# Kernel tuning notes

Measured on AMD Instinct MI355X. Metric: run time of the kernel, lower is better.

## Reference

```python
import jax, jax.numpy as jnp
import numpy as np

B = 16        # batch
N = 1024      # satellite nodes
D = 256       # hidden size
H = 8         # attention heads
NUM_LAYERS = 3          # config.n_layer_aa
L = NUM_LAYERS + 1      # distinct GAT layers
EPS = 1e-5


def setup_inputs() -> dict:
    key = jax.random.key(0)
    ks = jax.random.split(key, 6)
    graph_vectors = jax.random.normal(ks[0], (B, N + 1, D), dtype=jnp.float32)
    graph = jax.random.uniform(ks[1], (B, N, N), dtype=jnp.float32)
    scale = 0.02
    Wq = jax.random.normal(ks[2], (L, D, D), dtype=jnp.float32) * scale
    Wk = jax.random.normal(ks[3], (L, D, D), dtype=jnp.float32) * scale
    Wv = jax.random.normal(ks[4], (L, D, D), dtype=jnp.float32) * scale
    Wo = jax.random.normal(ks[5], (L, D, D), dtype=jnp.float32) * scale
    ln_g = jnp.ones((L, D), dtype=jnp.float32)
    ln_b = jnp.zeros((L, D), dtype=jnp.float32)
    return {"graph_vectors": graph_vectors, "graph": graph,
            "Wq": Wq, "Wk": Wk, "Wv": Wv, "Wo": Wo,
            "ln_g": ln_g, "ln_b": ln_b}


def _layer_norm(x, g, b):
    mu = jnp.mean(x, axis=-1, keepdims=True)
    var = jnp.var(x, axis=-1, keepdims=True)
    return (x - mu) * jax.lax.rsqrt(var + EPS) * g + b


def _gat(x_q, x_kv, wq, wk, wv, wo, g, b):
    # multi-head attention: x_q [B,Lq,D] attends over x_kv [B,Lk,D]
    Bq, Lq, _ = x_q.shape
    Lk = x_kv.shape[1]
    dh = D // H
    q = (x_q @ wq).reshape(Bq, Lq, H, dh)
    k = (x_kv @ wk).reshape(Bq, Lk, H, dh)
    v = (x_kv @ wv).reshape(Bq, Lk, H, dh)
    scores = jnp.einsum('bqhd,bkhd->bhqk', q, k) / jnp.sqrt(jnp.float32(dh))
    attn = jax.nn.softmax(scores, axis=-1)
    o = jnp.einsum('bhqk,bkhd->bqhd', attn, v).reshape(Bq, Lq, D)
    out = o @ wo
    return _layer_norm(out + x_q, g, b)


def reference(graph_vectors, graph, Wq, Wk, Wv, Wo, ln_g, ln_b):
    relay = graph_vectors[:, :1, :]        # [B,1,D]
    sat = graph_vectors[:, 1:, :]          # [B,N,D]
    # layer 0: relay attends over satellites
    relay = _gat(relay, sat, Wq[0], Wk[0], Wv[0], Wo[0], ln_g[0], ln_b[0])
    # satellite = (satellite^T @ graph)^T -> [B,N,D]
    sat = jnp.einsum('bnd,bnm->bmd', sat, graph)
    gv = jnp.concatenate([relay, sat], axis=1)   # [B,N+1,D]
    # middle layers: full self-attention over all N+1 nodes
    for i in range(1, NUM_LAYERS):
        gv = _gat(gv, gv, Wq[i], Wk[i], Wv[i], Wo[i], ln_g[i], ln_b[i])
    relay_u = gv[:, :1, :]
    sat_u = gv[:, 1:, :]
    z = _gat(relay_u, sat_u, Wq[-1], Wk[-1], Wv[-1], Wo[-1], ln_g[-1], ln_b[-1])[:, 0, :]
    return z, sat_u
```

## Files before the change

### kernel.cpp

```cpp
#include <hip/hip_runtime.h>
#include <hip/hip_bf16.h>
#include <math.h>

#define BD   256
#define NH   8
#define DH   32
#define NB   16
#define NN   1024
#define LQ   1025
#define EPSV 1e-5f
#define KP   1088

typedef unsigned short ushort_t;
typedef __attribute__((ext_vector_type(8))) short short8;
typedef __attribute__((ext_vector_type(4))) float f32x4;

static __device__ __forceinline__ ushort_t f2b(float x) {
  union { __hip_bfloat16 h; ushort_t u; } cv;
  cv.h = __float2bfloat16(x);
  return cv.u;
}
static __device__ __forceinline__ float b2f(ushort_t u) {
  union { float f; unsigned v; } c; c.v = ((unsigned)u) << 16; return c.f;
}
static __device__ __forceinline__ float fexp2(float x) {
#if defined(__has_builtin)
#if __has_builtin(__builtin_amdgcn_exp2f)
  return __builtin_amdgcn_exp2f(x);
#else
  return exp2f(x);
#endif
#else
  return exp2f(x);
#endif
}

__global__ void k_copy_cast(const float* __restrict__ in, float* __restrict__ X,
                            ushort_t* __restrict__ Xh, long n) {
  long stride = (long)gridDim.x * 256;
  for (long i = (long)blockIdx.x * 256 + threadIdx.x; i < n; i += stride) {
    float v = in[i];
    X[i] = v;
    Xh[i] = f2b(v);
  }
}

__global__ void k_sat_out(const float* __restrict__ X, float* __restrict__ out) {
  long n = (long)NB * NN * BD;
  long stride = (long)gridDim.x * 256;
  for (long i = (long)blockIdx.x * 256 + threadIdx.x; i < n; i += stride) {
    long b = i / ((long)NN * BD);
    long r = i - b * ((long)NN * BD);
    out[i] = X[b * (long)LQ * BD + BD + r];
  }
}

__global__ __launch_bounds__(256) void k_wtrans(const float* __restrict__ Wq,
                                                const float* __restrict__ Wk,
                                                const float* __restrict__ Wv,
                                                const float* __restrict__ Wo,
                                                ushort_t* __restrict__ Wt) {
  const float C1 = 0.17677669529663687f * 1.4426950408889634f;
  int mat = blockIdx.y;
  int type = mat >> 2, layer = mat & 3;
  const float* src = (type == 0) ? Wq : (type == 1) ? Wk : (type == 2) ? Wv : Wo;
  src += (long)layer * BD * BD;
  float scv = (type == 0) ? C1 : 1.f;
  ushort_t* dst = Wt + (long)mat * BD * BD;
  __shared__ float t[32][33];
  int k0 = (blockIdx.x & 7) * 32, n0 = (blockIdx.x >> 3) * 32;
  int tid = threadIdx.x;
  for (int i = tid; i < 1024; i += 256) {
    int kk = i >> 5, nn = i & 31;
    t[kk][nn] = src[(long)(k0 + kk) * BD + n0 + nn];
  }
  __syncthreads();
  for (int i = tid; i < 1024; i += 256) {
    int nn = i >> 5, kk = i & 31;
    dst[(long)(n0 + nn) * BD + k0 + kk] = f2b(t[kk][nn] * scv);
  }
}

__global__ __launch_bounds__(256) void k_gtrans(const float* __restrict__ G,
                                                ushort_t* __restrict__ Ght) {
  __shared__ ushort_t t[64][65];
  int b = blockIdx.y;
  int m0 = (blockIdx.x & 15) * 64, n0 = (blockIdx.x >> 4) * 64;
  const float* Gb = G + (long)b * NN * NN;
  ushort_t* dst = Ght + (long)b * NN * NN;
  int tid = threadIdx.x;
  #pragma unroll
  for (int rr = 0; rr < 16; rr++) {
    int n = rr * 4 + (tid >> 6);
    int m = tid & 63;
    t[m][n] = f2b(Gb[(long)(n0 + n) * NN + m0 + m]);
  }
  __syncthreads();
  #pragma unroll
  for (int rr = 0; rr < 8; rr++) {
    int m = rr * 8 + (tid >> 5);
    int n2 = (tid & 31) * 2;
    unsigned w = (unsigned)t[m][n2] | ((unsigned)t[m][n2 + 1] << 16);
    *(unsigned*)&dst[(long)(m0 + m) * NN + n0 + n2] = w;
  }
}

__global__ __launch_bounds__(256) void k_satT(const ushort_t* __restrict__ Xh,
                                              ushort_t* __restrict__ satT) {
  __shared__ ushort_t t[64][65];
  int b = blockIdx.y;
  int n0 = (blockIdx.x & 15) * 64, d0 = (blockIdx.x >> 4) * 64;
  const ushort_t* src = Xh + ((long)b * LQ + 1) * BD;
  ushort_t* dst = satT + (long)b * BD * NN;
  int tid = threadIdx.x;
  #pragma unroll
  for (int rr = 0; rr < 16; rr++) {
    int n = rr * 4 + (tid >> 6);
    int d = tid & 63;
    t[n][d] = src[(long)(n0 + n) * BD + d0 + d];
  }
  __syncthreads();
  #pragma unroll
  for (int rr = 0; rr < 8; rr++) {
    int d = rr * 8 + (tid >> 5);
    int n2 = (tid & 31) * 2;
    unsigned w = (unsigned)t[n2][d] | ((unsigned)t[n2 + 1][d] << 16);
    *(unsigned*)&dst[(long)(d0 + d) * NN + n0 + n2] = w;
  }
}

__global__ __launch_bounds__(256) void k_vtrans(const ushort_t* __restrict__ Vh,
                                                ushort_t* __restrict__ VhT) {
  __shared__ ushort_t t[64][65];
  int b = blockIdx.z;
  int n0 = blockIdx.x * 64, d0 = blockIdx.y * 64;
  const ushort_t* src = Vh + (long)b * LQ * BD;
  ushort_t* dst = VhT + (long)b * BD * KP;
  int tid = threadIdx.x;
  #pragma unroll
  for (int rr = 0; rr < 16; rr++) {
    int n = rr * 4 + (tid >> 6);
    int d = tid & 63;
    int key = n0 + n;
    t[n][d] = (key < LQ) ? src[(long)key * BD + d0 + d] : (ushort_t)0;
  }
  __syncthreads();
  #pragma unroll
  for (int rr = 0; rr < 8; rr++) {
    int d = rr * 8 + (tid >> 5);
    int n2 = (tid & 31) * 2;
    unsigned w = (unsigned)t[n2][d] | ((unsigned)t[n2 + 1][d] << 16);
    *(unsigned*)&dst[(long)(d0 + d) * KP + n0 + n2] = w;
  }
}

static __device__ __forceinline__ void gemm_core(const ushort_t* __restrict__ A,
                                                 const ushort_t* __restrict__ W,
                                                 ushort_t* Ws,
                                                 float* __restrict__ Cf,
                                                 ushort_t* __restrict__ Ch,
                                                 int M, int m0, int n0) {
  int tid = threadIdx.x;
  int wave = tid >> 6, lane = tid & 63;
  int l15 = lane & 15, quad = lane >> 4;
  for (int i = tid; i < 64 * 32; i += 256) {
    int r = i >> 5, c8 = (i & 31) * 8;
    *(uint4*)&Ws[r * 264 + c8] = *(const uint4*)&W[(long)(n0 + r) * 256 + c8];
  }
  __syncthreads();
  int mrow = m0 + wave * 16 + l15;
  if (mrow > M - 1) mrow = M - 1;
  f32x4 acc[4];
  #pragma unroll
  for (int f = 0; f < 4; f++) { acc[f][0] = 0.f; acc[f][1] = 0.f; acc[f][2] = 0.f; acc[f][3] = 0.f; }
  #pragma unroll
  for (int k0 = 0; k0 < 256; k0 += 32) {
    short8 a = *(const short8*)&A[(long)mrow * 256 + k0 + quad * 8];
    #pragma unroll
    for (int f = 0; f < 4; f++) {
      short8 bb = *(const short8*)&Ws[(f * 16 + l15) * 264 + k0 + quad * 8];
      acc[f] = __builtin_amdgcn_mfma_f32_16x16x32_bf16(a, bb, acc[f], 0, 0, 0);
    }
  }
  #pragma unroll
  for (int f = 0; f < 4; f++)
    #pragma unroll
    for (int r = 0; r < 4; r++) {
      int m = m0 + wave * 16 + quad * 4 + r;
      if (m < M) {
        long idx = (long)m * 256 + n0 + f * 16 + l15;
        if (Cf) Cf[idx] = acc[f][r];
        else    Ch[idx] = f2b(acc[f][r]);
      }
    }
}

__global__ __launch_bounds__(256) void gemm_qkv(const ushort_t* __restrict__ Xh,
                                                const ushort_t* __restrict__ Wt, int layer,
                                                ushort_t* __restrict__ Qo,
                                                ushort_t* __restrict__ Ko,
                                                ushort_t* __restrict__ Vo, int M) {
  __shared__ __align__(16) ushort_t Ws[64 * 264];
  int which = blockIdx.y >> 2, n0 = (blockIdx.y & 3) * 64;
  const ushort_t* W = Wt + (long)(which * 4 + layer) * 65536;
  ushort_t* C = (which == 0) ? Qo : (which == 1) ? Ko : Vo;
  gemm_core(Xh, W, Ws, nullptr, C, M, blockIdx.x * 64, n0);
}

__global__ __launch_bounds__(256) void gemm_kv(const ushort_t* __restrict__ Xh,
                                               const ushort_t* __restrict__ Wt, int layer,
                                               ushort_t* __restrict__ Ko,
                                               ushort_t* __restrict__ Vo) {
  __shared__ __align__(16) ushort_t Ws[64 * 264];
  int which = blockIdx.y >> 2, n0 = (blockIdx.y & 3) * 64;
  int b = blockIdx.z;
  const ushort_t* W = Wt + (long)((which + 1) * 4 + layer) * 65536;
  const ushort_t* A = Xh + (long)b * (LQ * BD) + BD;
  ushort_t* C = ((which == 0) ? Ko : Vo) + (long)b * (NN * BD);
  gemm_core(A, W, Ws, nullptr, C, NN, blockIdx.x * 64, n0);
}

__global__ __launch_bounds__(256) void gemm_oproj(const ushort_t* __restrict__ Oh,
                                                  const ushort_t* __restrict__ Wt, int layer,
                                                  float* __restrict__ Cf, int M) {
  __shared__ __align__(16) ushort_t Ws[64 * 264];
  gemm_core(Oh, Wt + (long)(12 + layer) * 65536, Ws, Cf, nullptr, M,
            blockIdx.x * 64, blockIdx.y * 64);
}

__global__ __launch_bounds__(256) void gemm_gtx2(const ushort_t* __restrict__ Ght,
                                                 const ushort_t* __restrict__ satT,
                                                 float* __restrict__ X,
                                                 ushort_t* __restrict__ Xh) {
  int b = blockIdx.z;
  const ushort_t* A = Ght + (long)b * NN * NN;
  const ushort_t* Bp = satT + (long)b * BD * NN;
  int tid = threadIdx.x;
  int wave = tid >> 6, lane = tid & 63;
  int l15 = lane & 15, quad = lane >> 4;
  int m0 = blockIdx.x * 64, d0 = blockIdx.y * 64;
  int arow = m0 + wave * 16 + l15;
  f32x4 acc[4];
  #pragma unroll
  for (int f = 0; f < 4; f++) { acc[f][0] = 0.f; acc[f][1] = 0.f; acc[f][2] = 0.f; acc[f][3] = 0.f; }
  for (int n0 = 0; n0 < NN; n0 += 32) {
    short8 a = *(const short8*)&A[(long)arow * NN + n0 + quad * 8];
    #pragma unroll
    for (int f = 0; f < 4; f++) {
      short8 bb = *(const short8*)&Bp[(long)(d0 + f * 16 + l15) * NN + n0 + quad * 8];
      acc[f] = __builtin_amdgcn_mfma_f32_16x16x32_bf16(a, bb, acc[f], 0, 0, 0);
    }
  }
  long xb = ((long)b * LQ + 1) * 256;
  #pragma unroll
  for (int f = 0; f < 4; f++)
    #pragma unroll
    for (int r = 0; r < 4; r++) {
      int m = m0 + wave * 16 + quad * 4 + r;
      int d = d0 + f * 16 + l15;
      long idx = xb + (long)m * 256 + d;
      X[idx] = acc[f][r];
      Xh[idx] = f2b(acc[f][r]);
    }
}

__global__ __launch_bounds__(256) void attn_fa(const ushort_t* __restrict__ Qh,
                                               const ushort_t* __restrict__ Kh,
                                               const ushort_t* __restrict__ VhT,
                                               ushort_t* __restrict__ Oh) {
  __shared__ __align__(16) ushort_t Ps[4][32][72];
  __shared__ __align__(16) ushort_t Kb[64 * 72];
  __shared__ __align__(16) ushort_t Vb[32 * 72];
  __shared__ float Lbuf[4][32];
  int tid = threadIdx.x;
  int wave = tid >> 6, lane = tid & 63;
  int l15 = lane & 15, quad = lane >> 4;
  int b = blockIdx.x >> 3, h = blockIdx.x & 7;
  long hb = ((long)b * LQ) * BD + h * DH;
  long vB = (long)b * BD * KP;
  int hd0 = h * DH;
  int q0 = blockIdx.y * 128 + wave * 32;
  int lq = lane & 48;

  short8 qB[2];
  #pragma unroll
  for (int t = 0; t < 2; t++) {
    int qc = q0 + t * 16 + l15; if (qc > LQ - 1) qc = LQ - 1;
    qB[t] = *(const short8*)&Qh[hb + (long)qc * BD + quad * 8];
  }

  const ushort_t *s0, *s1;
  ushort_t *d0, *d1;
  long stp;
  if (wave < 2) {
    int kt0 = wave * 2, kt1 = kt0 + 1;
    s0 = Kh + hb + (long)(kt0 * 16 + l15) * BD + quad * 8;
    s1 = Kh + hb + (long)(kt1 * 16 + l15) * BD + quad * 8;
    d0 = &Kb[(kt0 * 16 + l15) * 72 + quad * 8];
    d1 = &Kb[(kt1 * 16 + l15) * 72 + quad * 8];
    stp = (long)64 * BD;
  } else {
    int sa = (wave - 2) * 2, sb = sa + 1;
    s0 = VhT + vB + (long)(hd0 + (sa >> 1) * 16 + l15) * KP + (sa & 1) * 32 + quad * 8;
    s1 = VhT + vB + (long)(hd0 + (sb >> 1) * 16 + l15) * KP + (sb & 1) * 32 + quad * 8;
    d0 = &Vb[((sa >> 1) * 16 + l15) * 72 + (sa & 1) * 32 + quad * 8];
    d1 = &Vb[((sb >> 1) * 16 + l15) * 72 + (sb & 1) * 32 + quad * 8];
    stp = 64;
  }
  {
    uint4 r0 = *(const uint4*)s0;
    uint4 r1 = *(const uint4*)s1;
    *(uint4*)d0 = r0;
    *(uint4*)d1 = r1;
  }
  __syncthreads();

  f32x4 o[2][2];
  #pragma unroll
  for (int t = 0; t < 2; t++)
    #pragma unroll
    for (int dt = 0; dt < 2; dt++) { o[t][dt][0] = 0.f; o[t][dt][1] = 0.f; o[t][dt][2] = 0.f; o[t][dt][3] = 0.f; }
  float m[2] = {-1e30f, -1e30f};
  float ls[2] = {0.f, 0.f};
  f32x4 zf; zf[0] = 0.f; zf[1] = 0.f; zf[2] = 0.f; zf[3] = 0.f;

  for (int c = 0; c < 17; c++) {
    bool more = (c < 16);
    uint4 n0, n1;
    if (more) {
      if (c == 15 && wave < 2) {
        const ushort_t* cl = Kh + hb + (long)(LQ - 1) * BD + quad * 8;
        n0 = *(const uint4*)cl;
        n1 = n0;
      } else {
        s0 += stp; s1 += stp;
        n0 = *(const uint4*)s0;
        n1 = *(const uint4*)s1;
      }
    }
    short8 ka[4];
    #pragma unroll
    for (int kt = 0; kt < 4; kt++)
      ka[kt] = *(const short8*)&Kb[(kt * 16 + l15) * 72 + quad * 8];

    bool tail = (c == 16);
    #pragma unroll
    for (int t = 0; t < 2; t++) {
      f32x4 s[4];
      #pragma unroll
      for (int kt = 0; kt < 4; kt++)
        s[kt] = __builtin_amdgcn_mfma_f32_16x16x32_bf16(ka[kt], qB[t], zf, 0, 0, 0);
      if (tail) {
        #pragma unroll
        for (int kt = 0; kt < 4; kt++)
          #pragma unroll
          for (int r = 0; r < 4; r++)
            if (kt + r) s[kt][r] = -1e30f;
        if (quad) s[0][0] = -1e30f;
      }
      float cm = fmaxf(fmaxf(s[0][0], s[0][1]), fmaxf(s[0][2], s[0][3]));
      cm = fmaxf(cm, fmaxf(fmaxf(s[1][0], s[1][1]), fmaxf(s[1][2], s[1][3])));
      cm = fmaxf(cm, fmaxf(fmaxf(s[2][0], s[2][1]), fmaxf(s[2][2], s[2][3])));
      cm = fmaxf(cm, fmaxf(fmaxf(s[3][0], s[3][1]), fmaxf(s[3][2], s[3][3])));
      cm = fmaxf(cm, __shfl_xor(cm, 16));
      cm = fmaxf(cm, __shfl_xor(cm, 32));
      if (__any(cm > m[t] + 8.f)) {
        float mn = fmaxf(m[t], cm);
        float f = fexp2(m[t] - mn);
        ls[t] *= f;
        m[t] = mn;
        #pragma unroll
        for (int r = 0; r < 4; r++) {
          float fr = __shfl(f, lq | (quad * 4 + r));
          o[t][0][r] *= fr;
          o[t][1][r] *= fr;
        }
      }
      float mt = m[t];
      #pragma unroll
      for (int kt = 0; kt < 4; kt++) {
        float p0 = fexp2(s[kt][0] - mt);
        float p1 = fexp2(s[kt][1] - mt);
        float p2 = fexp2(s[kt][2] - mt);
        float p3 = fexp2(s[kt][3] - mt);
        ls[t] += (p0 + p1) + (p2 + p3);
        unsigned lo = (unsigned)f2b(p0) | ((unsigned)f2b(p1) << 16);
        unsigned hi = (unsigned)f2b(p2) | ((unsigned)f2b(p3) << 16);
        uint2 w; w.x = lo; w.y = hi;
        *(uint2*)&Ps[wave][t * 16 + l15][kt * 16 + quad * 4] = w;
      }
    }
    short8 vb[2][2];
    #pragma unroll
    for (int dt = 0; dt < 2; dt++)
      #pragma unroll
      for (int ks = 0; ks < 2; ks++)
        vb[ks][dt] = *(const short8*)&Vb[(dt * 16 + l15) * 72 + ks * 32 + quad * 8];
    #pragma unroll
    for (int ks = 0; ks < 2; ks++) {
      short8 pa0 = *(const short8*)&Ps[wave][l15][ks * 32 + quad * 8];
      short8 pa1 = *(const short8*)&Ps[wave][16 + l15][ks * 32 + quad * 8];
      #pragma unroll
      for (int dt = 0; dt < 2; dt++) {
        o[0][dt] = __builtin_amdgcn_mfma_f32_16x16x32_bf16(pa0, vb[ks][dt], o[0][dt], 0, 0, 0);
        o[1][dt] = __builtin_amdgcn_mfma_f32_16x16x32_bf16(pa1, vb[ks][dt], o[1][dt], 0, 0, 0);
      }
    }
    if (more) {
      __syncthreads();
      *(uint4*)d0 = n0;
      *(uint4*)d1 = n1;
      __syncthreads();
    }
  }
  #pragma unroll
  for (int t = 0; t < 2; t++) {
    ls[t] += __shfl_xor(ls[t], 16);
    ls[t] += __shfl_xor(ls[t], 32);
  }
  if (quad == 0) {
    Lbuf[wave][l15] = ls[0];
    Lbuf[wave][16 + l15] = ls[1];
  }
  __syncthreads();
  #pragma unroll
  for (int mt = 0; mt < 2; mt++) {
    f32x4 lv = *(const f32x4*)&Lbuf[wave][mt * 16 + quad * 4];
    #pragma unroll
    for (int r = 0; r < 4; r++) {
      int row = q0 + mt * 16 + quad * 4 + r;
      if (row < LQ) {
        float den = lv[r];
        float inv = (den > 0.f) ? 1.f / den : 0.f;
        #pragma unroll
        for (int dt = 0; dt < 2; dt++)
          Oh[hb + (long)row * BD + dt * 16 + l15] = f2b(o[mt][dt][r] * inv);
      }
    }
  }
}

__global__ __launch_bounds__(256) void attn_relay(const float* __restrict__ q,
                                                  const ushort_t* __restrict__ K,
                                                  const ushort_t* __restrict__ V,
                                                  float* __restrict__ o) {
  int b = blockIdx.x, h = blockIdx.y;
  int tid = threadIdx.x;
  const float scale = 0.17677669529663687f;
  __shared__ float s[NN];
  __shared__ float qs[DH];
  __shared__ float rbuf[256];
  __shared__ float part[8][33];
  if (tid < DH) qs[tid] = q[(long)b * BD + h * DH + tid];
  __syncthreads();
  long base = ((long)b * NN) * BD + h * DH;
  for (int k = tid; k < NN; k += 256) {
    float dot = 0.f;
    const ushort_t* kr = &K[base + (long)k * BD];
    #pragma unroll
    for (int d2 = 0; d2 < 16; d2++) {
      unsigned w = *(const unsigned*)&kr[d2 * 2];
      dot += qs[d2 * 2] * b2f((ushort_t)(w & 0xffff)) + qs[d2 * 2 + 1] * b2f((ushort_t)(w >> 16));
    }
    s[k] = dot * scale;
  }
  __syncthreads();
  float m = -1e30f;
  for (int k = tid; k < NN; k += 256) m = fmaxf(m, s[k]);
  rbuf[tid] = m;
  __syncthreads();
  for (int st = 128; st > 0; st >>= 1) {
    if (tid < st) rbuf[tid] = fmaxf(rbuf[tid], rbuf[tid + st]);
    __syncthreads();
  }
  float mx = rbuf[0];
  __syncthreads();
  float sm = 0.f;
  for (int k = tid; k < NN; k += 256) {
    float p = __expf(s[k] - mx);
    s[k] = p;
    sm += p;
  }
  rbuf[tid] = sm;
  __syncthreads();
  for (int st = 128; st > 0; st >>= 1) {
    if (tid < st) rbuf[tid] += rbuf[tid + st];
    __syncthreads();
  }
  float inv = 1.f / rbuf[0];
  int d = tid & 31, slice = tid >> 5;
  float acc = 0.f;
  for (int k = slice; k < NN; k += 8) acc += s[k] * b2f(V[base + (long)k * BD + d]);
  part[slice][d] = acc;
  __syncthreads();
  if (tid < DH) {
    float ss = 0.f;
    #pragma unroll
    for (int t = 0; t < 8; t++) ss += part[t][tid];
    o[(long)b * BD + h * DH + tid] = ss * inv;
  }
}

__global__ __launch_bounds__(256) void rowvec_matmul(const float* __restrict__ X, long xstride,
                                                     const float* __restrict__ W,
                                                     float* __restrict__ out) {
  int b = blockIdx.x, tid = threadIdx.x;
  __shared__ float xs[BD];
  xs[tid] = X[(long)b * xstride + tid];
  __syncthreads();
  float acc = 0.f;
  for (int k = 0; k < BD; k++) acc += xs[k] * W[(long)k * BD + tid];
  out[(long)b * BD + tid] = acc;
}

__global__ __launch_bounds__(256) void rowvec_oproj_ln(const float* __restrict__ o,
                                                       const float* __restrict__ Wo,
                                                       const float* __restrict__ Xres, long xstride,
                                                       const float* __restrict__ g,
                                                       const float* __restrict__ beta,
                                                       float* __restrict__ dst, long dstride,
                                                       ushort_t* __restrict__ dsth, long dhstride) {
  int b = blockIdx.x, tid = threadIdx.x;
  __shared__ float xs[BD];
  __shared__ float rs[256], rq[256];
  xs[tid] = o[(long)b * BD + tid];
  __syncthreads();
  float acc = 0.f;
  for (int k = 0; k < BD; k++) acc += xs[k] * Wo[(long)k * BD + tid];
  float v = acc + Xres[(long)b * xstride + tid];
  rs[tid] = v;
  rq[tid] = v * v;
  __syncthreads();
  for (int st = 128; st > 0; st >>= 1) {
    if (tid < st) { rs[tid] += rs[tid + st]; rq[tid] += rq[tid + st]; }
    __syncthreads();
  }
  float mu = rs[0] * (1.f / BD);
  float var = rq[0] * (1.f / BD) - mu * mu;
  float y = (v - mu) * rsqrtf(var + EPSV) * g[tid] + beta[tid];
  dst[(long)b * dstride + tid] = y;
  if (dsth) dsth[(long)b * dhstride + tid] = f2b(y);
}

__global__ __launch_bounds__(256) void ln_residual(const float* __restrict__ OP,
                                                   float* __restrict__ X,
                                                   ushort_t* __restrict__ Xh,
                                                   const float* __restrict__ g,
                                                   const float* __restrict__ beta) {
  long r = blockIdx.x;
  int tid = threadIdx.x;
  __shared__ float rs[256], rq[256];
  float v = OP[r * BD + tid] + X[r * BD + tid];
  rs[tid] = v;
  rq[tid] = v * v;
  __syncthreads();
  for (int st = 128; st > 0; st >>= 1) {
    if (tid < st) { rs[tid] += rs[tid + st]; rq[tid] += rq[tid + st]; }
    __syncthreads();
  }
  float mu = rs[0] * (1.f / BD);
  float var = rq[0] * (1.f / BD) - mu * mu;
  float y = (v - mu) * rsqrtf(var + EPSV) * g[tid] + beta[tid];
  X[r * BD + tid] = y;
  Xh[r * BD + tid] = f2b(y);
}

extern "C" void kernel_launch(void* const* d_in, const int* in_sizes, int n_in,
                              void* d_out, int out_size, void* d_ws, size_t ws_size,
                              hipStream_t stream) {
  const float* gv    = (const float*)d_in[0];
  const float* graph = (const float*)d_in[1];
  const float* Wq    = (const float*)d_in[2];
  const float* Wk    = (const float*)d_in[3];
  const float* Wv    = (const float*)d_in[4];
  const float* Wo    = (const float*)d_in[5];
  const float* lg    = (const float*)d_in[6];
  const float* lb    = (const float*)d_in[7];
  float* out = (float*)d_out;

  const long S  = (long)NB * LQ * BD;
  const long S4 = S * 4, S2 = S * 2;
  char* base = (char*)d_ws;
  float*    X    = (float*)base;
  ushort_t* Xh   = (ushort_t*)(base + S4);
  float*    B1   = (float*)(base + S4 + S2);
  ushort_t* Qh   = (ushort_t*)(base + 2 * S4 + S2);
  ushort_t* Kh   = (ushort_t*)(base + 2 * S4 + 2 * S2);
  ushort_t* Vh   = (ushort_t*)(base + 2 * S4 + 3 * S2);
  ushort_t* Oh   = (ushort_t*)(base + 2 * S4 + 4 * S2);
  ushort_t* Wt   = (ushort_t*)(base + 2 * S4 + 5 * S2);
  float*    qrel = (float*)(base + 2 * S4 + 5 * S2 + 16L * 65536 * 2);
  float*    orel = qrel + (long)NB * BD;
  ushort_t* Ght  = (ushort_t*)B1;
  ushort_t* satT = Vh;
  ushort_t* VhT  = (ushort_t*)B1;

  const long WSZ = (long)BD * BD;
  const long XST = (long)LQ * BD;
  dim3 blk(256);

  k_copy_cast<<<dim3(2048), blk, 0, stream>>>(gv, X, Xh, S);
  k_wtrans<<<dim3(64, 16), blk, 0, stream>>>(Wq, Wk, Wv, Wo, Wt);

  rowvec_matmul<<<dim3(NB), blk, 0, stream>>>(X, XST, Wq + 0 * WSZ, qrel);
  gemm_kv<<<dim3(16, 8, NB), blk, 0, stream>>>(Xh, Wt, 0, Kh, Vh);
  attn_relay<<<dim3(NB, NH), blk, 0, stream>>>(qrel, Kh, Vh, orel);
  rowvec_oproj_ln<<<dim3(NB), blk, 0, stream>>>(orel, Wo + 0 * WSZ, X, XST,
                                                lg + 0 * BD, lb + 0 * BD, X, XST, Xh, XST);

  k_gtrans<<<dim3(256, NB), blk, 0, stream>>>(graph, Ght);
  k_satT<<<dim3(64, NB), blk, 0, stream>>>(Xh, satT);
  gemm_gtx2<<<dim3(16, 4, NB), blk, 0, stream>>>(Ght, satT, X, Xh);

  for (int l = 1; l <= 2; l++) {
    gemm_qkv<<<dim3(257, 12), blk, 0, stream>>>(Xh, Wt, l, Qh, Kh, Vh, NB * LQ);
    k_vtrans<<<dim3(17, 4, NB), blk, 0, stream>>>(Vh, VhT);
    attn_fa<<<dim3(NB * NH, 9), blk, 0, stream>>>(Qh, Kh, VhT, Oh);
    gemm_oproj<<<dim3(257, 4), blk, 0, stream>>>(Oh, Wt, l, B1, NB * LQ);
    ln_residual<<<dim3(NB * LQ), blk, 0, stream>>>(B1, X, Xh, lg + l * BD, lb + l * BD);
  }

  k_sat_out<<<dim3(2048), blk, 0, stream>>>(X, out + (long)NB * BD);

  rowvec_matmul<<<dim3(NB), blk, 0, stream>>>(X, XST, Wq + 3 * WSZ, qrel);
  gemm_kv<<<dim3(16, 8, NB), blk, 0, stream>>>(Xh, Wt, 3, Kh, Vh);
  attn_relay<<<dim3(NB, NH), blk, 0, stream>>>(qrel, Kh, Vh, orel);
  rowvec_oproj_ln<<<dim3(NB), blk, 0, stream>>>(orel, Wo + 3 * WSZ, X, XST,
                                                lg + 3 * BD, lb + 3 * BD, out, BD, nullptr, 0);
}
```

Measured before the change: 600.4 us.

## Tile graph-propagation GEMM through LDS with 128x128 blocks and register prefetch

The graph-times-satellite GEMM previously streamed A and B fragments straight from global memory per wave, so each block reused little data. It now stages 128x128 A/B tiles in shared memory, gives each wave a 64x64 output sub-tile (4x4 MFMA accumulators), and prefetches the next K-slice into registers while computing the current one. The grid shrinks from 16x4 to 8x2 blocks per batch, which cuts global traffic but lowers block count and raises register use.

```diff
diff --git a/kernel.cpp b/kernel.cpp
--- a/kernel.cpp
+++ b/kernel.cpp
@@ -232,36 +232,88 @@
                                                  const ushort_t* __restrict__ satT,
                                                  float* __restrict__ X,
                                                  ushort_t* __restrict__ Xh) {
+  __shared__ __align__(16) ushort_t As[128 * 72];
+  __shared__ __align__(16) ushort_t Bs[128 * 72];
   int b = blockIdx.z;
-  const ushort_t* A = Ght + (long)b * NN * NN;
+  const ushort_t* A  = Ght + (long)b * NN * NN;
   const ushort_t* Bp = satT + (long)b * BD * NN;
   int tid = threadIdx.x;
   int wave = tid >> 6, lane = tid & 63;
   int l15 = lane & 15, quad = lane >> 4;
-  int m0 = blockIdx.x * 64, d0 = blockIdx.y * 64;
-  int arow = m0 + wave * 16 + l15;
-  f32x4 acc[4];
-  #pragma unroll
-  for (int f = 0; f < 4; f++) { acc[f][0] = 0.f; acc[f][1] = 0.f; acc[f][2] = 0.f; acc[f][3] = 0.f; }
-  for (int n0 = 0; n0 < NN; n0 += 32) {
-    short8 a = *(const short8*)&A[(long)arow * NN + n0 + quad * 8];
-    #pragma unroll
-    for (int f = 0; f < 4; f++) {
-      short8 bb = *(const short8*)&Bp[(long)(d0 + f * 16 + l15) * NN + n0 + quad * 8];
-      acc[f] = __builtin_amdgcn_mfma_f32_16x16x32_bf16(a, bb, acc[f], 0, 0, 0);
-    }
-  }
+  int wr = wave >> 1, wc = wave & 1;
+  int m0 = blockIdx.x * 128, d0 = blockIdx.y * 128;
+
+  int sr = tid >> 2, sc = (tid & 3) * 8;
+  const ushort_t* aSrc0 = A  + (long)(m0 + sr) * NN + sc;
+  const ushort_t* aSrc1 = aSrc0 + (long)64 * NN;
+  const ushort_t* bSrc0 = Bp + (long)(d0 + sr) * NN + sc;
+  const ushort_t* bSrc1 = bSrc0 + (long)64 * NN;
+  ushort_t* aDst0 = &As[sr * 72 + sc];
+  ushort_t* aDst1 = aDst0 + 64 * 72;
+  ushort_t* bDst0 = &Bs[sr * 72 + sc];
+  ushort_t* bDst1 = bDst0 + 64 * 72;
+
+  {
+    uint4 a0 = *(const uint4*)aSrc0;
+    uint4 a1 = *(const uint4*)aSrc1;
+    uint4 b0 = *(const uint4*)bSrc0;
+    uint4 b1 = *(const uint4*)bSrc1;
+    *(uint4*)aDst0 = a0; *(uint4*)aDst1 = a1;
+    *(uint4*)bDst0 = b0; *(uint4*)bDst1 = b1;
+  }
+  __syncthreads();
+
+  f32x4 acc[4][4];
+  #pragma unroll
+  for (int i = 0; i < 4; i++)
+    #pragma unroll
+    for (int j = 0; j < 4; j++) { acc[i][j][0] = 0.f; acc[i][j][1] = 0.f; acc[i][j][2] = 0.f; acc[i][j][3] = 0.f; }
+
+  for (int ks = 0; ks < 32; ks++) {
+    bool more = (ks < 31);
+    uint4 na0, na1, nb0, nb1;
+    if (more) {
+      aSrc0 += 32; aSrc1 += 32; bSrc0 += 32; bSrc1 += 32;
+      na0 = *(const uint4*)aSrc0;
+      na1 = *(const uint4*)aSrc1;
+      nb0 = *(const uint4*)bSrc0;
+      nb1 = *(const uint4*)bSrc1;
+    }
+    short8 af[4], bf[4];
+    #pragma unroll
+    for (int f = 0; f < 4; f++)
+      af[f] = *(const short8*)&As[(wr * 64 + f * 16 + l15) * 72 + quad * 8];
+    #pragma unroll
+    for (int f = 0; f < 4; f++)
+      bf[f] = *(const short8*)&Bs[(wc * 64 + f * 16 + l15) * 72 + quad * 8];
+    #pragma unroll
+    for (int i = 0; i < 4; i++)
+      #pragma unroll
+      for (int j = 0; j < 4; j++)
+        acc[i][j] = __builtin_amdgcn_mfma_f32_16x16x32_bf16(af[i], bf[j], acc[i][j], 0, 0, 0);
+    if (more) {
+      __syncthreads();
+      *(uint4*)aDst0 = na0;
+      *(uint4*)aDst1 = na1;
+      *(uint4*)bDst0 = nb0;
+      *(uint4*)bDst1 = nb1;
+      __syncthreads();
+    }
+  }
+
   long xb = ((long)b * LQ + 1) * 256;
   #pragma unroll
-  for (int f = 0; f < 4; f++)
-    #pragma unroll
-    for (int r = 0; r < 4; r++) {
-      int m = m0 + wave * 16 + quad * 4 + r;
-      int d = d0 + f * 16 + l15;
-      long idx = xb + (long)m * 256 + d;
-      X[idx] = acc[f][r];
-      Xh[idx] = f2b(acc[f][r]);
-    }
+  for (int i = 0; i < 4; i++)
+    #pragma unroll
+    for (int j = 0; j < 4; j++)
+      #pragma unroll
+      for (int r = 0; r < 4; r++) {
+        int m = m0 + wr * 64 + i * 16 + quad * 4 + r;
+        int d = d0 + wc * 64 + j * 16 + l15;
+        long idx = xb + (long)m * 256 + d;
+        X[idx] = acc[i][j][r];
+        Xh[idx] = f2b(acc[i][j][r]);
+      }
 }
 
 __global__ __launch_bounds__(256) void attn_fa(const ushort_t* __restrict__ Qh,
@@ -610,7 +662,7 @@
 
   k_gtrans<<<dim3(256, NB), blk, 0, stream>>>(graph, Ght);
   k_satT<<<dim3(64, NB), blk, 0, stream>>>(Xh, satT);
-  gemm_gtx2<<<dim3(16, 4, NB), blk, 0, stream>>>(Ght, satT, X, Xh);
+  gemm_gtx2<<<dim3(8, 2, NB), blk, 0, stream>>>(Ght, satT, X, Xh);
 
   for (int l = 1; l <= 2; l++) {
     gemm_qkv<<<dim3(257, 12), blk, 0, stream>>>(Xh, Wt, l, Qh, Kh, Vh, NB * LQ);
```

After: 553.6 us. 7.8% less time.
